# Optimization experiments

Hardware: AMD Instinct MI355X
Metric: run time of the kernel (lower is better)

Reference implementation:

```python
import jax, jax.numpy as jnp
import numpy as np

B, FEW, NN = 4096, 5, 64
D = 128            # embed_dim
NSYM = 100000
DM = 2 * D         # d_model = 256
DI = 2 * DM        # support-encoder inner = 512
H = 2 * DM         # LSTMCell hidden = 512
STEPS = 4          # process_steps


def setup_inputs() -> dict:
    key = jax.random.key(0)
    cnt = [0]
    def nk():
        cnt[0] += 1
        return jax.random.fold_in(key, cnt[0])
    def nrm(shape, scale=0.05):
        return jax.random.normal(nk(), shape, dtype=jnp.float32) * scale
    def ridx(shape):
        return jax.random.randint(nk(), shape, 0, NSYM, dtype=jnp.int32)
    inp = {}
    inp['q_l1'] = ridx((B, NN, 2)); inp['q_l2'] = ridx((B, NN, 2))
    inp['q_r1'] = ridx((B, NN, 2)); inp['q_r2'] = ridx((B, NN, 2))
    inp['s_l1'] = ridx((FEW, NN, 2)); inp['s_l2'] = ridx((FEW, NN, 2))
    inp['s_r1'] = ridx((FEW, NN, 2)); inp['s_r2'] = ridx((FEW, NN, 2))
    inp['q_deg_l'] = jax.random.randint(nk(), (B,), 1, NN, dtype=jnp.int32)
    inp['q_deg_r'] = jax.random.randint(nk(), (B,), 1, NN, dtype=jnp.int32)
    inp['s_deg_l'] = jax.random.randint(nk(), (FEW,), 1, NN, dtype=jnp.int32)
    inp['s_deg_r'] = jax.random.randint(nk(), (FEW,), 1, NN, dtype=jnp.int32)
    inp['emb'] = nrm((NSYM + 1, D)).at[NSYM].set(0.0)  # padding_idx row = 0
    inp['gcn_w'] = nrm((D, 2 * D))
    inp['gcn_wb'] = nrm((D,))
    inp['gcn_b'] = jnp.zeros((D,), jnp.float32)
    inp['hop_gate'] = jnp.ones((2,), jnp.float32)
    inp['attn_w'] = nrm((1, D))
    inp['attn_b'] = jnp.zeros((1,), jnp.float32)
    inp['p1_w'] = nrm((DI, DM)); inp['p1_b'] = jnp.zeros((DI,), jnp.float32)
    inp['p2_w'] = nrm((DM, DI)); inp['p2_b'] = jnp.zeros((DM,), jnp.float32)
    inp['ln_g'] = jnp.ones((DM,), jnp.float32); inp['ln_b'] = jnp.zeros((DM,), jnp.float32)
    inp['w_ih'] = nrm((4 * H, DM)); inp['w_hh'] = nrm((4 * H, H))
    inp['b_ih'] = jnp.zeros((4 * H,), jnp.float32); inp['b_hh'] = jnp.zeros((4 * H,), jnp.float32)
    return inp


def _neighbor_encoder(conn, emb, gcn_w, gcn_wb, gcn_b, attn_w, attn_b):
    # conn: [N, NN, 2] (relation id, entity id)
    e = emb[conn]                                     # [N, NN, 2, D]
    concat = e.reshape(conn.shape[0], conn.shape[1], 2 * D)  # cat(rel, ent)
    proj = concat @ gcn_w.T + gcn_wb + gcn_b          # [N, NN, D]
    scores = (proj @ attn_w.T + attn_b)[..., 0]       # [N, NN]
    w = jax.nn.softmax(scores, axis=1)[..., None]
    return jnp.tanh(jnp.sum(proj * w, axis=1))        # [N, D]


def _support_encoder(x, p1_w, p1_b, p2_w, p2_b, ln_g, ln_b):
    out = jax.nn.relu(x @ p1_w.T + p1_b) @ p2_w.T + p2_b
    z = out + x
    mu = jnp.mean(z, axis=-1, keepdims=True)
    var = jnp.var(z, axis=-1, keepdims=True)
    return (z - mu) / jnp.sqrt(var + 1e-6) * ln_g + ln_b


def _query_encoder(support_g, q, w_ih, w_hh, b_ih, b_hh):
    # matching-networks 'process' LSTM attention, STEPS fixed iterations
    h_r = jnp.zeros((q.shape[0], H), q.dtype)
    c = jnp.zeros_like(h_r)
    h = q
    for _ in range(STEPS):
        gates = q @ w_ih.T + b_ih + h_r @ w_hh.T + b_hh
        i, f, g, o = jnp.split(gates, 4, axis=-1)
        c = jax.nn.sigmoid(f) * c + jax.nn.sigmoid(i) * jnp.tanh(g)
        h_cell = jax.nn.sigmoid(o) * jnp.tanh(c)
        h = q + h_cell[:, :DM]
        attn = jax.nn.softmax(h @ support_g.T, axis=1)
        r = attn @ support_g
        h_r = jnp.concatenate([h, r], axis=1)
    return h


def reference(q_l1, q_l2, q_r1, q_r2, s_l1, s_l2, s_r1, s_r2,
              q_deg_l, q_deg_r, s_deg_l, s_deg_r,
              emb, gcn_w, gcn_wb, gcn_b, hop_gate, attn_w, attn_b,
              p1_w, p1_b, p2_w, p2_b, ln_g, ln_b, w_ih, w_hh, b_ih, b_hh):
    ne = lambda conn: _neighbor_encoder(conn, emb, gcn_w, gcn_wb, gcn_b, attn_w, attn_b)
    gw = jax.nn.softmax(hop_gate)
    q_left = gw[0] * ne(q_l1) + gw[1] * ne(q_l2)
    q_right = gw[0] * ne(q_r1) + gw[1] * ne(q_r2)
    s_left = gw[0] * ne(s_l1) + gw[1] * ne(s_l2)
    s_right = gw[0] * ne(s_r1) + gw[1] * ne(s_r2)
    query_neighbor = jnp.concatenate([q_left, q_right], axis=-1)    # [B, DM]
    support_neighbor = jnp.concatenate([s_left, s_right], axis=-1)  # [FEW, DM]
    support_g = _support_encoder(support_neighbor, p1_w, p1_b, p2_w, p2_b, ln_g, ln_b)
    query_g = _query_encoder(support_g, query_neighbor, w_ih, w_hh, b_ih, b_hh)
    support_m = jnp.mean(support_g, axis=0, keepdims=True)          # [1, DM]
    return (query_g @ support_m.T)[:, 0]                            # [B]
```

## Files before the change

kernel.cpp:

```cpp
#include <hip/hip_runtime.h>

typedef unsigned short bf16u;
typedef unsigned char u8;
typedef unsigned int u32;
typedef float f32x4 __attribute__((ext_vector_type(4)));
typedef short bf16x8 __attribute__((ext_vector_type(8)));

__device__ inline float sigmoidf_(float x) { return 1.f / (1.f + __expf(-x)); }
__device__ inline float tanhf_(float x) {
  float e = __expf(2.f * x);
  return 1.f - 2.f / (e + 1.f);
}
__device__ inline float b2f(bf16u u) { return __uint_as_float(((u32)u) << 16); }
__device__ inline bf16u f2b(float f) {
  u32 i = __float_as_uint(f);
  u32 r = (i + 0x7fffu + ((i >> 16) & 1u)) >> 16;
  return (bf16u)r;
}
__device__ inline u8 enc8(float v) {
  float q = fmaf(v, 512.f, 128.5f);
  q = fminf(fmaxf(q, 0.f), 255.f);
  return (u8)(int)q;
}
__device__ inline float ub0(u32 u) { return (float)(u & 0xffu); }
__device__ inline float ub1(u32 u) { return (float)((u >> 8) & 0xffu); }
__device__ inline float ub2(u32 u) { return (float)((u >> 16) & 0xffu); }
__device__ inline float ub3(u32 u) { return (float)(u >> 24); }

#define GLOAD16(gsrc, ldst)                                                   \
  __builtin_amdgcn_global_load_lds(                                           \
      (const __attribute__((address_space(1))) void*)(gsrc),                  \
      (__attribute__((address_space(3))) void*)(ldst), 16, 0, 0)

__global__ __launch_bounds__(256) void k_vprep(
    const float* __restrict__ gcn_w, bf16u* __restrict__ Vp)
{
  const int g = blockIdx.x * 256 + threadIdx.x;
  const int half = g >> 11, rem = g & 2047;
  const int r = rem >> 4, qs = rem & 15;
  const int ls = qs ^ (r & 15);
  const float* src = gcn_w + r * 256 + half * 128 + ls * 8;
  float4 v0 = *(const float4*)src;
  float4 v1 = *(const float4*)(src + 4);
  ushort4 p0, p1;
  p0.x = f2b(v0.x); p0.y = f2b(v0.y); p0.z = f2b(v0.z); p0.w = f2b(v0.w);
  p1.x = f2b(v1.x); p1.y = f2b(v1.y); p1.z = f2b(v1.z); p1.w = f2b(v1.w);
  *(ushort4*)(Vp + (size_t)g * 8) = p0;
  *(ushort4*)(Vp + (size_t)g * 8 + 4) = p1;
}

__global__ __launch_bounds__(256) void k_front(
    const float* __restrict__ emb, const bf16u* __restrict__ Vp,
    const float* __restrict__ attn_w,
    const float* __restrict__ w_ih, const float* __restrict__ w_hh,
    const float* __restrict__ b_ih, const float* __restrict__ b_hh,
    u8* __restrict__ pr, u8* __restrict__ pe,
    float* __restrict__ srel, float* __restrict__ sent,
    bf16u* __restrict__ WWa, bf16u* __restrict__ WWb, float* __restrict__ bsum,
    bf16u* __restrict__ XX)
{
  const int blk = blockIdx.x, t = threadIdx.x;
  if (blk >= 1563) {
    const int b = blk - 1563;
    if (t < 59) {
      XX[(size_t)b * 576 + 517 + t] = 0;
      XX[(size_t)(b + 2048) * 576 + 517 + t] = 0;
    }
    float wi = w_ih[b * 256 + t];
    float wh = w_hh[b * 512 + t];
    WWa[(size_t)b * 576 + t] = f2b(wi);
    WWb[(size_t)b * 576 + t] = f2b(wi + wh);
    WWb[(size_t)b * 576 + 256 + t] = f2b(wh);
    if (t < 59) WWb[(size_t)b * 576 + 517 + t] = 0;
    if (t == 0) bsum[b] = b_ih[b] + b_hh[b];
    return;
  }
  const int row0 = blk << 6;
  __shared__ short As[64][136];
  __shared__ union PB {
    short B[128][128];
    u8 ob[64][272];
  } pb;
  __shared__ float scp[2][2][64];

  const int wave = t >> 6, lane = t & 63;
  const int quad = lane >> 4, l16 = lane & 15;
  const int wm = (wave >> 1) << 5, wn = (wave & 1) << 6;

  {
    char* lbase = (char*)&pb.B[0][0] + wave * 8192;
    #pragma unroll
    for (int e = 0; e < 8; ++e) {
      int s = wave * 512 + e * 64 + lane;
      GLOAD16(Vp + (size_t)s * 8, lbase + e * 1024);
    }
  }
  #pragma unroll
  for (int s = 0; s < 8; ++s) {
    int f = s * 256 + t;
    int row = f >> 5, q = f & 31;
    int gr = row0 + row; if (gr > 100000) gr = 100000;
    float4 v = *(const float4*)&emb[(size_t)gr * 128 + (q << 2)];
    ushort4 pk;
    pk.x = f2b(v.x); pk.y = f2b(v.y); pk.z = f2b(v.z); pk.w = f2b(v.w);
    *(ushort4*)&As[row][q << 2] = pk;
  }
  float aw[4];
  #pragma unroll
  for (int j = 0; j < 4; ++j) aw[j] = attn_w[wn + j * 16 + l16];

  f32x4 acc0[2][4], acc1[2][4];
  #pragma unroll
  for (int i = 0; i < 2; ++i)
    #pragma unroll
    for (int j = 0; j < 4; ++j) {
      acc0[i][j] = (f32x4){0.f, 0.f, 0.f, 0.f};
      acc1[i][j] = (f32x4){0.f, 0.f, 0.f, 0.f};
    }
  __syncthreads();
  #pragma unroll
  for (int kc = 0; kc < 4; ++kc) {
    bf16x8 af[2], bfr[4];
    #pragma unroll
    for (int i = 0; i < 2; ++i)
      af[i] = *(const bf16x8*)&As[wm + i * 16 + l16][kc * 32 + quad * 8];
    #pragma unroll
    for (int j = 0; j < 4; ++j)
      bfr[j] = *(const bf16x8*)&pb.B[wn + j * 16 + l16]
                                    [((kc * 4 + quad) ^ l16) * 8];
    #pragma unroll
    for (int i = 0; i < 2; ++i)
      #pragma unroll
      for (int j = 0; j < 4; ++j)
        acc0[i][j] = __builtin_amdgcn_mfma_f32_16x16x32_bf16(af[i], bfr[j], acc0[i][j], 0, 0, 0);
  }
  __syncthreads();
  {
    char* lbase = (char*)&pb.B[0][0] + wave * 8192;
    #pragma unroll
    for (int e = 0; e < 8; ++e) {
      int s = wave * 512 + e * 64 + lane;
      GLOAD16(Vp + 16384 + (size_t)s * 8, lbase + e * 1024);
    }
  }
  __syncthreads();
  #pragma unroll
  for (int kc = 0; kc < 4; ++kc) {
    bf16x8 af[2], bfr[4];
    #pragma unroll
    for (int i = 0; i < 2; ++i)
      af[i] = *(const bf16x8*)&As[wm + i * 16 + l16][kc * 32 + quad * 8];
    #pragma unroll
    for (int j = 0; j < 4; ++j)
      bfr[j] = *(const bf16x8*)&pb.B[wn + j * 16 + l16]
                                    [((kc * 4 + quad) ^ l16) * 8];
    #pragma unroll
    for (int i = 0; i < 2; ++i)
      #pragma unroll
      for (int j = 0; j < 4; ++j)
        acc1[i][j] = __builtin_amdgcn_mfma_f32_16x16x32_bf16(af[i], bfr[j], acc1[i][j], 0, 0, 0);
  }
  {
    #pragma unroll
    for (int i = 0; i < 2; ++i) {
      #pragma unroll
      for (int r = 0; r < 4; ++r) {
        float t0 = acc0[i][0][r] * aw[0] + acc0[i][1][r] * aw[1] +
                   acc0[i][2][r] * aw[2] + acc0[i][3][r] * aw[3];
        float t1 = acc1[i][0][r] * aw[0] + acc1[i][1][r] * aw[1] +
                   acc1[i][2][r] * aw[2] + acc1[i][3][r] * aw[3];
        #pragma unroll
        for (int m = 1; m < 16; m <<= 1) {
          t0 += __shfl_xor(t0, m, 64);
          t1 += __shfl_xor(t1, m, 64);
        }
        if (l16 == 0) {
          int row = wm + i * 16 + quad * 4 + r;
          scp[0][wn >> 6][row] = t0;
          scp[1][wn >> 6][row] = t1;
        }
      }
    }
  }
  __syncthreads();
  #pragma unroll
  for (int j = 0; j < 4; ++j) {
    const int col = wn + j * 16 + l16;
    #pragma unroll
    for (int i = 0; i < 2; ++i) {
      #pragma unroll
      for (int r = 0; r < 4; ++r) {
        int row = wm + i * 16 + quad * 4 + r;
        pb.ob[row][col] = enc8(acc0[i][j][r]);
        pb.ob[row][128 + col] = enc8(acc1[i][j][r]);
      }
    }
  }
  if (t < 64) {
    int gr = row0 + t;
    if (gr <= 100000) {
      srel[gr] = scp[0][0][t] + scp[0][1][t];
      sent[gr] = scp[1][0][t] + scp[1][1][t];
    }
  }
  __syncthreads();
  #pragma unroll
  for (int s = 0; s < 4; ++s) {
    int c = s * 256 + t;
    int row = c >> 4, part = c & 15;
    int gr = row0 + row;
    if (gr <= 100000) {
      uint4 v = *(const uint4*)&pb.ob[row][part * 16];
      if (part < 8) *(uint4*)&pr[(size_t)gr * 128 + part * 16] = v;
      else          *(uint4*)&pe[(size_t)gr * 128 + (part - 8) * 16] = v;
    }
  }
}

__global__ __launch_bounds__(256) void k_neighbor(
    const int* __restrict__ q_l1, const int* __restrict__ q_l2,
    const int* __restrict__ q_r1, const int* __restrict__ q_r2,
    const int* __restrict__ s_l1, const int* __restrict__ s_l2,
    const int* __restrict__ s_r1, const int* __restrict__ s_r2,
    const u8* __restrict__ pr, const u8* __restrict__ pe,
    const float* __restrict__ srel, const float* __restrict__ sent,
    const float* __restrict__ gcn_wb, const float* __restrict__ gcn_b,
    const float* __restrict__ hop_gate,
    float* __restrict__ qn, float* __restrict__ sn, bf16u* __restrict__ XX)
{
  const int b = blockIdx.x, t = threadIdx.x;
  const int *cA, *cB; float* outp; bf16u* xxp; int n, coloff;
  if (b < 4096)      { cA = q_l1; cB = q_l2; n = b;        outp = qn; xxp = XX; coloff = 0; }
  else if (b < 8192) { cA = q_r1; cB = q_r2; n = b - 4096; outp = qn; xxp = XX; coloff = 128; }
  else if (b < 8197) { cA = s_l1; cB = s_l2; n = b - 8192; outp = sn; xxp = 0;  coloff = 0; }
  else               { cA = s_r1; cB = s_r2; n = b - 8197; outp = sn; xxp = 0;  coloff = 128; }

  __shared__ float wS[2][64];
  __shared__ float red[256][17];

  const int hop = t >> 7, g = (t >> 3) & 15, p = t & 7;
  const int* connG = hop ? cB : cA;

  int2 pairs[4];
  #pragma unroll
  for (int kk = 0; kk < 4; ++kk)
    pairs[kk] = *(const int2*)&connG[(n * 64 + g + (kk << 4)) * 2];

  float vR = 0.f, vE = 0.f;
  if (t < 128) {
    const int sh = t >> 6, nn = t & 63;
    const int* connS = sh ? cB : cA;
    int2 sp = *(const int2*)&connS[(n * 64 + nn) * 2];
    vR = srel[sp.x];
    vE = sent[sp.y];
  }

  uint4 ra[4], rb[4];
  #pragma unroll
  for (int kk = 0; kk < 4; ++kk) {
    ra[kk] = *(const uint4*)&pr[(size_t)pairs[kk].x * 128 + p * 16];
    rb[kk] = *(const uint4*)&pe[(size_t)pairs[kk].y * 128 + p * 16];
  }

  if (t < 128) {
    const int sh = t >> 6, nn = t & 63;
    float sc = vR + vE;
    float m = sc;
    #pragma unroll
    for (int off = 32; off; off >>= 1) m = fmaxf(m, __shfl_xor(m, off, 64));
    float e = __expf(sc - m);
    float s = e;
    #pragma unroll
    for (int off = 32; off; off >>= 1) s += __shfl_xor(s, off, 64);
    wS[sh][nn] = e / s;
  }
  __syncthreads();

  float a[16];
  #pragma unroll
  for (int c = 0; c < 16; ++c) a[c] = 0.f;
  #pragma unroll
  for (int kk = 0; kk < 4; ++kk) {
    const float wk = wS[hop][g + (kk << 4)];
    const uint4 A = ra[kk], Bv = rb[kk];
    a[0]  += wk * (ub0(A.x) + ub0(Bv.x));
    a[1]  += wk * (ub1(A.x) + ub1(Bv.x));
    a[2]  += wk * (ub2(A.x) + ub2(Bv.x));
    a[3]  += wk * (ub3(A.x) + ub3(Bv.x));
    a[4]  += wk * (ub0(A.y) + ub0(Bv.y));
    a[5]  += wk * (ub1(A.y) + ub1(Bv.y));
    a[6]  += wk * (ub2(A.y) + ub2(Bv.y));
    a[7]  += wk * (ub3(A.y) + ub3(Bv.y));
    a[8]  += wk * (ub0(A.z) + ub0(Bv.z));
    a[9]  += wk * (ub1(A.z) + ub1(Bv.z));
    a[10] += wk * (ub2(A.z) + ub2(Bv.z));
    a[11] += wk * (ub3(A.z) + ub3(Bv.z));
    a[12] += wk * (ub0(A.w) + ub0(Bv.w));
    a[13] += wk * (ub1(A.w) + ub1(Bv.w));
    a[14] += wk * (ub2(A.w) + ub2(Bv.w));
    a[15] += wk * (ub3(A.w) + ub3(Bv.w));
  }
  #pragma unroll
  for (int c = 0; c < 16; ++c) red[t][c] = a[c];
  __syncthreads();

  if (t < 128) {
    const int d = t, pp = d >> 4, cc = d & 15;
    float sA = 0.f, sB = 0.f;
    #pragma unroll
    for (int gg = 0; gg < 16; ++gg) {
      sA += red[gg * 8 + pp][cc];
      sB += red[128 + gg * 8 + pp][cc];
    }
    float accA = sA * (1.f / 512.f) - 0.5f;
    float accB = sB * (1.f / 512.f) - 0.5f;
    float bias = gcn_wb[d] + gcn_b[d];
    float g0 = hop_gate[0], g1 = hop_gate[1];
    float mx = fmaxf(g0, g1);
    float e0 = __expf(g0 - mx), e1 = __expf(g1 - mx);
    float inv = 1.f / (e0 + e1);
    float v = e0 * inv * tanhf_(bias + accA) + e1 * inv * tanhf_(bias + accB);
    outp[n * 256 + coloff + d] = v;
    if (xxp) xxp[(size_t)n * 576 + coloff + d] = f2b(v);
  }
}

__global__ __launch_bounds__(256) void k_sup1(
    const float* __restrict__ sn, const float* __restrict__ p1_w,
    const float* __restrict__ p1_b, float* __restrict__ h1)
{
  const int r = blockIdx.x >> 3, j0 = (blockIdx.x & 7) << 6;
  const int t = threadIdx.x;
  __shared__ float xs[256];
  xs[t] = sn[r * 256 + t];
  __syncthreads();
  const int j = j0 + (t >> 2), q = t & 3;
  const float* wr = p1_w + (size_t)j * 256 + q * 64;
  float acc = 0.f;
  #pragma unroll
  for (int k = 0; k < 64; ++k) acc += xs[q * 64 + k] * wr[k];
  acc += __shfl_xor(acc, 1, 64);
  acc += __shfl_xor(acc, 2, 64);
  if (q == 0) h1[r * 512 + j] = fmaxf(acc + p1_b[j], 0.f);
}

__global__ __launch_bounds__(256) void k_sup2(
    const float* __restrict__ sn, const float* __restrict__ h1,
    const float* __restrict__ p2_w, const float* __restrict__ p2_b,
    const float* __restrict__ ln_g, const float* __restrict__ ln_b,
    float* __restrict__ sg)
{
  const int r = blockIdx.x, t = threadIdx.x;
  const int lane = t & 63, wave = t >> 6;
  __shared__ float hs[512];
  __shared__ float zs[256];
  __shared__ float r1[4], r2[4];
  hs[t] = h1[r * 512 + t];
  hs[t + 256] = h1[r * 512 + 256 + t];
  __syncthreads();
  const int q = t & 3;
  #pragma unroll
  for (int jc = 0; jc < 4; ++jc) {
    int j = jc * 64 + (t >> 2);
    const float* wr = p2_w + (size_t)j * 512 + q * 128;
    float acc = 0.f;
    #pragma unroll
    for (int k = 0; k < 128; ++k) acc += hs[q * 128 + k] * wr[k];
    acc += __shfl_xor(acc, 1, 64);
    acc += __shfl_xor(acc, 2, 64);
    if (q == 0) zs[j] = acc + p2_b[j] + sn[r * 256 + j];
  }
  __syncthreads();
  float v = zs[t];
  float s1 = v, s2 = v * v;
  #pragma unroll
  for (int off = 32; off; off >>= 1) { s1 += __shfl_xor(s1, off, 64); s2 += __shfl_xor(s2, off, 64); }
  if (lane == 0) { r1[wave] = s1; r2[wave] = s2; }
  __syncthreads();
  float S1 = r1[0] + r1[1] + r1[2] + r1[3];
  float S2 = r2[0] + r2[1] + r2[2] + r2[3];
  float mu = S1 * (1.f / 256.f);
  float var = S2 * (1.f / 256.f) - mu * mu;
  sg[r * 256 + t] = (v - mu) * rsqrtf(var + 1e-6f) * ln_g[t] + ln_b[t];
}

__global__ __launch_bounds__(256) void k_gates_mfma(
    const bf16u* __restrict__ XX, const bf16u* __restrict__ WW,
    const float* __restrict__ bsum, bf16u* __restrict__ gates, int kchunks,
    const float* __restrict__ sg, const float* __restrict__ w_hh,
    bf16u* __restrict__ WWbo, float* __restrict__ sm, int dosg2)
{
  const int t = threadIdx.x;
  const int wave = t >> 6, lane = t & 63;
  const int quad = lane >> 4, l16 = lane & 15;
  const int wm = (wave >> 1) << 6, wn = (wave & 1) << 6;
  const int lin = (blockIdx.x & 7) * 56 + (blockIdx.x >> 3);
  const int row0 = (lin / 14) << 7;
  const int col0 = (lin % 14) << 7;
  __shared__ short As[2][128][64];
  __shared__ short Bs[2][128][64];

  if (dosg2 && blockIdx.x < 32) {
    float (*s5)[256] = (float(*)[256])&As[0][0][0];
    const int blk = blockIdx.x;
    for (int i = t; i < 1280; i += 256) s5[i >> 8][i & 255] = sg[i];
    __syncthreads();
    if (blk == 0)
      sm[t] = (s5[0][t] + s5[1][t] + s5[2][t] + s5[3][t] + s5[4][t]) * 0.2f;
    const int j = (blk << 6) + (t >> 2), q = t & 3;
    const float4* wr = (const float4*)(w_hh + (size_t)j * 512 + 256 + q * 64);
    float a[5] = {0.f, 0.f, 0.f, 0.f, 0.f};
    #pragma unroll
    for (int kk = 0; kk < 16; ++kk) {
      float4 w = wr[kk];
      int k = q * 64 + kk * 4;
      #pragma unroll
      for (int r = 0; r < 5; ++r)
        a[r] += s5[r][k] * w.x + s5[r][k+1] * w.y + s5[r][k+2] * w.z + s5[r][k+3] * w.w;
    }
    #pragma unroll
    for (int r = 0; r < 5; ++r) {
      a[r] += __shfl_xor(a[r], 1, 64);
      a[r] += __shfl_xor(a[r], 2, 64);
    }
    if (q == 0) {
      #pragma unroll
      for (int r = 0; r < 5; ++r)
        WWbo[(size_t)j * 576 + 512 + r] = f2b(a[r]);
    }
    __syncthreads();
  }

  f32x4 acc[4][4];
  #pragma unroll
  for (int i = 0; i < 4; ++i)
    #pragma unroll
    for (int j = 0; j < 4; ++j) acc[i][j] = (f32x4){0.f, 0.f, 0.f, 0.f};

  int offX[4], offW[4];
  #pragma unroll
  for (int e = 0; e < 4; ++e) {
    int row = wave * 32 + e * 8 + (lane >> 3);
    int sw = (lane & 7) ^ (lane >> 3);
    offX[e] = (row0 + row) * 576 + sw * 8;
    offW[e] = (col0 + row) * 576 + sw * 8;
  }
  char* aBase = (char*)&As[0][0][0] + wave * 4096;
  char* bBase = (char*)&Bs[0][0][0] + wave * 4096;

  #define STAGE(buf, kc)                                                      \
    {                                                                         \
      const int kof_ = (kc) * 64;                                             \
      _Pragma("unroll")                                                       \
      for (int e = 0; e < 4; ++e) {                                           \
        GLOAD16(XX + offX[e] + kof_, aBase + (buf) * 16384 + e * 1024);       \
        GLOAD16(WW + offW[e] + kof_, bBase + (buf) * 16384 + e * 1024);       \
      }                                                                       \
    }

  STAGE(0, 0);
  __syncthreads();

  for (int kc = 0; kc < kchunks; ++kc) {
    const int cur = kc & 1;
    if (kc + 1 < kchunks) STAGE(cur ^ 1, kc + 1);
    #pragma unroll
    for (int kc2 = 0; kc2 < 2; ++kc2) {
      bf16x8 af[4], bfr[4];
      #pragma unroll
      for (int i = 0; i < 4; ++i)
        af[i] = *(const bf16x8*)&As[cur][wm + i * 16 + l16]
                                       [(((kc2 << 2) + quad) ^ (l16 & 7)) << 3];
      #pragma unroll
      for (int j = 0; j < 4; ++j)
        bfr[j] = *(const bf16x8*)&Bs[cur][wn + j * 16 + l16]
                                        [(((kc2 << 2) + quad) ^ (l16 & 7)) << 3];
      #pragma unroll
      for (int i = 0; i < 4; ++i)
        #pragma unroll
        for (int j = 0; j < 4; ++j)
          acc[i][j] = __builtin_amdgcn_mfma_f32_16x16x32_bf16(af[i], bfr[j], acc[i][j], 0, 0, 0);
    }
    __syncthreads();
  }
  #undef STAGE

  #pragma unroll
  for (int j = 0; j < 4; ++j) {
    const int col = col0 + wn + j * 16 + l16;
    const float bs = bsum[col];
    #pragma unroll
    for (int i = 0; i < 4; ++i) {
      #pragma unroll
      for (int r = 0; r < 4; ++r) {
        int row = row0 + wm + i * 16 + quad * 4 + r;
        gates[(size_t)row * 2048 + col] = f2b(acc[i][j][r] + bs);
      }
    }
  }
}

__global__ __launch_bounds__(256) void k_cell(
    const bf16u* __restrict__ gates, const float* __restrict__ qn,
    float* __restrict__ c, bf16u* __restrict__ XX,
    const float* __restrict__ sg, const float* __restrict__ sm,
    float* __restrict__ out, int step)
{
  __shared__ float red[4][6];
  const int b = blockIdx.x, t = threadIdx.x;
  const int lane = t & 63, wave = t >> 6;
  const bf16u* g = gates + (size_t)b * 2048;
  float i0 = b2f(g[t]),       f0 = b2f(g[512 + t]), gg0 = b2f(g[1024 + t]), o0 = b2f(g[1536 + t]);
  float i1 = b2f(g[256 + t]), f1 = b2f(g[768 + t]), gg1 = b2f(g[1280 + t]);
  float co0 = step ? c[b * 512 + t] : 0.f;
  float co1 = step ? c[b * 512 + 256 + t] : 0.f;
  float c0 = sigmoidf_(f0) * co0 + sigmoidf_(i0) * tanhf_(gg0);
  float c1 = sigmoidf_(f1) * co1 + sigmoidf_(i1) * tanhf_(gg1);
  if (step < 3) {
    c[b * 512 + t] = c0;
    c[b * 512 + 256 + t] = c1;
  }
  float hcv = sigmoidf_(o0) * tanhf_(c0);
  float h = qn[b * 256 + t] + hcv;
  if (step < 3) {
    XX[(size_t)b * 576 + 256 + t] = f2b(hcv);
    float dots[5];
    #pragma unroll
    for (int s = 0; s < 5; ++s) dots[s] = h * sg[s * 256 + t];
    #pragma unroll
    for (int off = 32; off; off >>= 1) {
      #pragma unroll
      for (int s = 0; s < 5; ++s) dots[s] += __shfl_xor(dots[s], off, 64);
    }
    if (lane == 0) {
      #pragma unroll
      for (int s = 0; s < 5; ++s) red[wave][s] = dots[s];
    }
    __syncthreads();
    #pragma unroll
    for (int s = 0; s < 5; ++s)
      dots[s] = red[0][s] + red[1][s] + red[2][s] + red[3][s];
    float m = dots[0];
    #pragma unroll
    for (int s = 1; s < 5; ++s) m = fmaxf(m, dots[s]);
    float sum = 0.f;
    #pragma unroll
    for (int s = 0; s < 5; ++s) sum += __expf(dots[s] - m);
    if (t < 5) {
      float dv = (t == 1) ? dots[1] : (t == 2) ? dots[2] : (t == 3) ? dots[3]
               : (t == 4) ? dots[4] : dots[0];
      XX[(size_t)b * 576 + 512 + t] = f2b(__expf(dv - m) / sum);
    }
  } else {
    float v = h * sm[t];
    #pragma unroll
    for (int off = 32; off; off >>= 1) v += __shfl_xor(v, off, 64);
    if (lane == 0) red[wave][0] = v;
    __syncthreads();
    if (t == 0) out[b] = red[0][0] + red[1][0] + red[2][0] + red[3][0];
  }
}

extern "C" void kernel_launch(void* const* d_in, const int* in_sizes, int n_in,
                              void* d_out, int out_size, void* d_ws, size_t ws_size,
                              hipStream_t stream)
{
  (void)in_sizes; (void)n_in; (void)out_size; (void)ws_size;
  const int *q_l1 = (const int*)d_in[0], *q_l2 = (const int*)d_in[1];
  const int *q_r1 = (const int*)d_in[2], *q_r2 = (const int*)d_in[3];
  const int *s_l1 = (const int*)d_in[4], *s_l2 = (const int*)d_in[5];
  const int *s_r1 = (const int*)d_in[6], *s_r2 = (const int*)d_in[7];
  const float* emb      = (const float*)d_in[12];
  const float* gcn_w    = (const float*)d_in[13];
  const float* gcn_wb   = (const float*)d_in[14];
  const float* gcn_b    = (const float*)d_in[15];
  const float* hop_gate = (const float*)d_in[16];
  const float* attn_w   = (const float*)d_in[17];
  const float* p1_w = (const float*)d_in[19];
  const float* p1_b = (const float*)d_in[20];
  const float* p2_w = (const float*)d_in[21];
  const float* p2_b = (const float*)d_in[22];
  const float* ln_g = (const float*)d_in[23];
  const float* ln_b = (const float*)d_in[24];
  const float* w_ih = (const float*)d_in[25];
  const float* w_hh = (const float*)d_in[26];
  const float* b_ih = (const float*)d_in[27];
  const float* b_hh = (const float*)d_in[28];

  char* base = (char*)d_ws;
  size_t off = 0;
  auto alloc = [&](size_t bytes) -> char* {
    char* r = base + off;
    off = (off + bytes + 255) & ~(size_t)255;
    return r;
  };
  u8* pr       = (u8*)alloc(100001ull * 128);
  u8* pe       = (u8*)alloc(100001ull * 128);
  float* srel  = (float*)alloc(100001ull * 4);
  float* sent  = (float*)alloc(100001ull * 4);
  bf16u* Vp    = (bf16u*)alloc(2ull * 16384 * 2);
  float* qn    = (float*)alloc(4096ull * 256 * 4);
  float* sn    = (float*)alloc(5 * 256 * 4);
  float* sg    = (float*)alloc(5 * 256 * 4);
  float* sm    = (float*)alloc(256 * 4);
  float* h1b   = (float*)alloc(5 * 512 * 4);
  bf16u* XX    = (bf16u*)alloc(4096ull * 576 * 2);
  bf16u* WWa   = (bf16u*)alloc(2048ull * 576 * 2);
  bf16u* WWb   = (bf16u*)alloc(2048ull * 576 * 2);
  float* bsum  = (float*)alloc(2048 * 4);
  bf16u* gates = (bf16u*)alloc(4096ull * 2048 * 2);
  float* cbuf  = (float*)alloc(4096ull * 512 * 4);

  k_vprep<<<16, 256, 0, stream>>>(gcn_w, Vp);
  k_front<<<3611, 256, 0, stream>>>(emb, Vp, attn_w, w_ih, w_hh, b_ih, b_hh,
                                    pr, pe, srel, sent, WWa, WWb, bsum, XX);
  k_neighbor<<<8202, 256, 0, stream>>>(q_l1, q_l2, q_r1, q_r2, s_l1, s_l2, s_r1, s_r2,
                                       pr, pe, srel, sent, gcn_wb, gcn_b, hop_gate,
                                       qn, sn, XX);
  k_sup1<<<40, 256, 0, stream>>>(sn, p1_w, p1_b, h1b);
  k_sup2<<<5, 256, 0, stream>>>(sn, h1b, p2_w, p2_b, ln_g, ln_b, sg);

  for (int step = 0; step < 4; ++step) {
    if (step == 0)
      k_gates_mfma<<<448, 256, 0, stream>>>(XX, WWa, bsum, gates, 4,
                                            sg, w_hh, WWb, sm, 1);
    else
      k_gates_mfma<<<448, 256, 0, stream>>>(XX, WWb, bsum, gates, 9,
                                            sg, w_hh, WWb, sm, 0);
    k_cell<<<4096, 256, 0, stream>>>(gates, qn, cbuf, XX, sg, sm, (float*)d_out, step);
  }
}
```

Baseline: 324.6 us.

## Precompute the step-invariant input-gate GEMM part once and reuse it across LSTM steps

```diff
diff --git a/kernel.cpp b/kernel.cpp
--- a/kernel.cpp
+++ b/kernel.cpp
@@ -386,7 +386,9 @@
 
 __global__ __launch_bounds__(256) void k_gates_mfma(
     const bf16u* __restrict__ XX, const bf16u* __restrict__ WW,
-    const float* __restrict__ bsum, bf16u* __restrict__ gates, int kchunks,
+    const float* __restrict__ bsum, bf16u* __restrict__ gates,
+    int koff, int kchunks,
+    const float* __restrict__ g0in, float* __restrict__ g0out,
     const float* __restrict__ sg, const float* __restrict__ w_hh,
     bf16u* __restrict__ WWbo, float* __restrict__ sm, int dosg2)
 {
@@ -432,10 +434,25 @@
   }
 
   f32x4 acc[4][4];
-  #pragma unroll
-  for (int i = 0; i < 4; ++i)
-    #pragma unroll
-    for (int j = 0; j < 4; ++j) acc[i][j] = (f32x4){0.f, 0.f, 0.f, 0.f};
+  if (g0in) {
+    #pragma unroll
+    for (int j = 0; j < 4; ++j) {
+      const int col = col0 + wn + j * 16 + l16;
+      #pragma unroll
+      for (int i = 0; i < 4; ++i) {
+        #pragma unroll
+        for (int r = 0; r < 4; ++r) {
+          int row = row0 + wm + i * 16 + quad * 4 + r;
+          acc[i][j][r] = g0in[(size_t)row * 1792 + col];
+        }
+      }
+    }
+  } else {
+    #pragma unroll
+    for (int i = 0; i < 4; ++i)
+      #pragma unroll
+      for (int j = 0; j < 4; ++j) acc[i][j] = (f32x4){0.f, 0.f, 0.f, 0.f};
+  }
 
   int offX[4], offW[4];
   #pragma unroll
@@ -450,7 +467,7 @@
 
   #define STAGE(buf, kc)                                                      \
     {                                                                         \
-      const int kof_ = (kc) * 64;                                             \
+      const int kof_ = ((kc) + koff) * 64;                                    \
       _Pragma("unroll")                                                       \
       for (int e = 0; e < 4; ++e) {                                           \
         GLOAD16(XX + offX[e] + kof_, aBase + (buf) * 16384 + e * 1024);       \
@@ -485,16 +502,31 @@
   }
   #undef STAGE
 
-  #pragma unroll
-  for (int j = 0; j < 4; ++j) {
-    const int col = col0 + wn + j * 16 + l16;
-    const float bs = bsum[col];
-    #pragma unroll
-    for (int i = 0; i < 4; ++i) {
-      #pragma unroll
-      for (int r = 0; r < 4; ++r) {
-        int row = row0 + wm + i * 16 + quad * 4 + r;
-        gates[(size_t)row * 2048 + col] = f2b(acc[i][j][r] + bs);
+  if (g0out) {
+    #pragma unroll
+    for (int j = 0; j < 4; ++j) {
+      const int col = col0 + wn + j * 16 + l16;
+      #pragma unroll
+      for (int i = 0; i < 4; ++i) {
+        #pragma unroll
+        for (int r = 0; r < 4; ++r) {
+          int row = row0 + wm + i * 16 + quad * 4 + r;
+          g0out[(size_t)row * 1792 + col] = acc[i][j][r];
+        }
+      }
+    }
+  } else {
+    #pragma unroll
+    for (int j = 0; j < 4; ++j) {
+      const int col = col0 + wn + j * 16 + l16;
+      const float bs = bsum[col];
+      #pragma unroll
+      for (int i = 0; i < 4; ++i) {
+        #pragma unroll
+        for (int r = 0; r < 4; ++r) {
+          int row = row0 + wm + i * 16 + quad * 4 + r;
+          gates[(size_t)row * 2048 + col] = f2b(acc[i][j][r] + bs);
+        }
       }
     }
   }
@@ -610,6 +642,7 @@
   float* bsum  = (float*)alloc(2048 * 4);
   bf16u* gates = (bf16u*)alloc(4096ull * 2048 * 2);
   float* cbuf  = (float*)alloc(4096ull * 512 * 4);
+  float* G0    = (float*)alloc(4096ull * 1792 * 4);
 
   k_vprep<<<16, 256, 0, stream>>>(gcn_w, Vp);
   k_front<<<3611, 256, 0, stream>>>(emb, Vp, attn_w, w_ih, w_hh, b_ih, b_hh,
@@ -620,12 +653,17 @@
   k_sup1<<<40, 256, 0, stream>>>(sn, p1_w, p1_b, h1b);
   k_sup2<<<5, 256, 0, stream>>>(sn, h1b, p2_w, p2_b, ln_g, ln_b, sg);
 
+  k_gates_mfma<<<448, 256, 0, stream>>>(XX, WWb, bsum, gates, 0, 4,
+                                        nullptr, G0, sg, w_hh, WWb, sm, 1);
+
   for (int step = 0; step < 4; ++step) {
     if (step == 0)
-      k_gates_mfma<<<448, 256, 0, stream>>>(XX, WWa, bsum, gates, 4,
-                                            sg, w_hh, WWb, sm, 1);
+      k_gates_mfma<<<448, 256, 0, stream>>>(XX, WWa, bsum, gates, 0, 4,
+                                            nullptr, nullptr,
+                                            sg, w_hh, WWb, sm, 0);
     else
-      k_gates_mfma<<<448, 256, 0, stream>>>(XX, WWb, bsum, gates, 9,
+      k_gates_mfma<<<448, 256, 0, stream>>>(XX, WWb, bsum, gates, 4, 5,
+                                            G0, nullptr,
                                             sg, w_hh, WWb, sm, 0);
     k_cell<<<4096, 256, 0, stream>>>(gates, qn, cbuf, XX, sg, sm, (float*)d_out, step);
   }
```

Measured after the change: 334.6 us. +3.1%, slower.
